# Kernel tuning notes

Measured on AMD Instinct MI355X. Metric: run time of the kernel, lower is better.

## Reference

```python
import jax, jax.numpy as jnp
import numpy as np

M = 5            # Anderson history size
LAM = 1e-4       # Tikhonov regularization on the Gram matrix
MAX_ITER = 50
TOL = 1e-5
BETA = 1.0
ALPHA = 0.9      # damping


def anderson(f, x0, m=M, lam=LAM, max_iter=MAX_ITER, tol=TOL, beta=BETA):
    """Anderson acceleration for fixed-point iteration (faithful to torch ref).

    x0: [bsz, L]. Variable history size n=min(k,m) is handled by masking the
    (m+1)x(m+1) system: inactive slots get an identity row -> alpha_j = 0.
    """
    bsz, L = x0.shape
    dt = x0.dtype
    F0 = f(x0)
    F1 = f(F0)
    X = jnp.zeros((bsz, m, L), dt).at[:, 0].set(x0).at[:, 1].set(F0)
    Fh = jnp.zeros((bsz, m, L), dt).at[:, 0].set(F0).at[:, 1].set(F1)
    eye_m = jnp.eye(m, dtype=dt)

    def body(carry):
        k, X, Fh, _ = carry
        n = jnp.minimum(k, m)
        active = (jnp.arange(m) < n).astype(dt)          # [m]
        G = Fh - X                                        # inactive rows are zero
        Hc = jnp.einsum('bil,bjl->bij', G, G) + lam * eye_m
        m2 = active[:, None] * active[None, :]
        # zero out inactive rows/cols, put 1 on their diagonal (=> alpha_j = 0)
        Hc = Hc * m2 + eye_m * (1.0 - active)
        H = jnp.zeros((bsz, m + 1, m + 1), dt)
        H = H.at[:, 0, 1:].set(active).at[:, 1:, 0].set(active).at[:, 1:, 1:].set(Hc)
        y = jnp.zeros((bsz, m + 1, 1), dt).at[:, 0, 0].set(1.0)
        alpha_c = jnp.linalg.solve(H, y)[:, 1:, 0]        # [bsz, m]
        xnew = beta * jnp.einsum('bm,bml->bl', alpha_c, Fh) \
             + (1.0 - beta) * jnp.einsum('bm,bml->bl', alpha_c, X)
        slot = k % m
        X = X.at[:, slot].set(xnew)
        fnew = f(xnew)
        Fh = Fh.at[:, slot].set(fnew)
        res = jnp.linalg.norm(fnew - xnew) / (1e-5 + jnp.linalg.norm(fnew))
        return (k + 1, X, Fh, res)

    def cond(carry):
        k, _, _, res = carry
        return jnp.logical_and(k < max_iter, res >= tol)

    k, X, Fh, res = jax.lax.while_loop(
        cond, body, (jnp.array(2), X, Fh, jnp.array(np.inf, dt)))
    return X[:, (k - 1) % m]


def make_f(x, maskf, W, b, alpha):
    """Damped forward step: z -> softmax_ch((1-a)z + a*Conv(mask-inject(z)))."""
    bsz, C, H, Wd = x.shape

    def f(zflat):
        z = zflat.reshape(bsz, C, H, Wd)
        zm = z * (1.0 - maskf) + maskf * x               # inject observed parts
        lin = jax.lax.conv_general_dilated(
            zm, W, window_strides=(1, 1), padding='SAME',
            dimension_numbers=('NCHW', 'OIHW', 'NCHW')) + b[None, :, None, None]
        pre = (1.0 - alpha) * z + alpha * lin
        return jax.nn.softmax(pre, axis=1).reshape(bsz, -1)

    return f


def setup_inputs() -> dict:
    key = jax.random.key(0)
    k1, k2, k3 = jax.random.split(key, 3)
    bsz, C, H, Wd = 32, 128, 32, 32
    x = jax.random.normal(k1, (bsz, C, H, Wd), jnp.float32)
    mask = jax.random.randint(k2, (bsz, 1, H, Wd), 0, 2).astype(jnp.int32)
    W = jax.random.normal(k3, (C, C, 3, 3), jnp.float32) * 0.05  # keep map contractive
    b = jnp.zeros((C,), jnp.float32)
    return {"x": x, "W": W, "b": b, "mask": mask}


def reference(x, W, b, mask):
    bsz, C, H, Wd = x.shape
    maskf = mask.astype(x.dtype)
    f = make_f(x, maskf, W, b, ALPHA)
    # z_start = softmax(zeros) over channel dim -> uniform 1/C
    z0 = jnp.full((bsz, C * H * Wd), 1.0 / C, x.dtype)
    zstar = anderson(f, z0)
    zn = f(zstar)            # one extra step, as in the torch forward
    return zn                # [bsz, C*H*W]
```

## Files before the change

### kernel.cpp

```cpp
#include <hip/hip_runtime.h>


typedef unsigned short u16;
using short8 = __attribute__((ext_vector_type(8))) short;
using f32x4  = __attribute__((ext_vector_type(4))) float;

#define SLOT 4194304

struct Ctrl { int done; int last_slot; };

__device__ __forceinline__ u16 f2bf(float f) {
  unsigned u = __builtin_bit_cast(unsigned, f);
  unsigned r = (u + 0x7FFFu + ((u >> 16) & 1u)) >> 16;
  return (u16)r;
}
__device__ __forceinline__ float bf2f(u16 h) {
  unsigned u = ((unsigned)h) << 16;
  return __builtin_bit_cast(float, u);
}

__global__ void __launch_bounds__(256) k_prepw(const float* __restrict__ W,
    u16* __restrict__ Wb, Ctrl* ctrl) {
  if (blockIdx.x == 0 && threadIdx.x == 0) { ctrl->done = 0; ctrl->last_slot = 4; }
  int t = blockIdx.x * 256 + threadIdx.x;
  int o = t >> 14;
  int rem = t & 16383;
  int cout = rem >> 7, cin = rem & 127;
  float v = W[(size_t)cout * 1152 + (size_t)cin * 9 + o];
  Wb[(size_t)o * 16384 + (size_t)cout * 128 + cin] = f2bf(v);
}

__global__ void __launch_bounds__(256) k_prepx(const float* __restrict__ x,
    u16* __restrict__ xsw) {
  int t = blockIdx.x * 256 + threadIdx.x;
  int g = t >> 15, p = t & 32767;
  int nb = p >> 10, gp = p & 1023, px = p & 31;
  short8 xv;
#pragma unroll
  for (int u = 0; u < 8; ++u) {
    float v = x[(size_t)nb * 131072 + (size_t)(g * 8 + u) * 1024 + gp];
    xv[u] = (short)f2bf(v);
  }
  *(short8*)(xsw + (size_t)p * 128 + (size_t)((g ^ (px & 7)) << 3)) = xv;
}

__global__ void __launch_bounds__(256)
__attribute__((amdgpu_waves_per_eu(4, 4)))
k_iter(
    const int e,
    const u16* __restrict__ xsw, const int* __restrict__ mask_,
    const u16* __restrict__ Wb, const float* __restrict__ bias,
    float* __restrict__ Fhp, u16* __restrict__ FhH, u16* __restrict__ Gp,
    float* __restrict__ gram, float* __restrict__ gpart,
    float* __restrict__ resp, Ctrl* __restrict__ ctrl)
{
  __shared__ char smem[27776];
  char*  As       = smem;
  float* rowmax_s = (float*)(smem + 26112);
  float* rowsum_s = (float*)(smem + 26624);
  float* red      = (float*)(smem + 27136);
  float* alpha_s  = (float*)(smem + 27264);
  float* res_s    = (float*)(smem + 27284);
  int*   mk3      = (int*)(smem + 27392);

  if (ctrl->done) return;

  const int tid = threadIdx.x;
  const int wv = tid >> 6, lane = tid & 63;
  const int lhi = lane >> 4, llo = lane & 15;
  const int bhw = blockIdx.x;
  const int lbid = ((bhw & 7) << 7) + (bhw >> 3);
  const int n = lbid >> 5, y0 = lbid & 31;
  const int gpix0 = (n << 10) + (y0 << 5);
  const int slot = e % 5;
  const int nact = e < 5 ? e : 5;
  const size_t base = ((size_t)lbid * 256 + tid) * 16;

  if (e >= 3) {
    if (tid < 64) {
      float sd = 0.f, sf = 0.f;
      for (int i = tid; i < 1024; i += 64) { sd += resp[2 * i]; sf += resp[2 * i + 1]; }
#pragma unroll
      for (int off = 1; off < 64; off <<= 1) { sd += __shfl_xor(sd, off); sf += __shfl_xor(sf, off); }
      if (tid == 0) res_s[0] = sqrtf(sd) / (1e-5f + sqrtf(sf));
    }
    __syncthreads();
    if (res_s[0] < 1e-5f) {
      if (tid == 0) { ctrl->done = 1; ctrl->last_slot = (e - 1) % 5; }
      return;
    }
  }

  if (tid < 96) {
    int r = tid >> 5, xx = tid & 31;
    int gy = y0 - 1 + r;
    mk3[tid] = ((unsigned)gy < 32u) ? mask_[(n << 10) + (gy << 5) + xx] : 0;
  }
  if (e >= 1 && tid >= 96 && tid < 101) {
    int j = tid - 96;
    float s = 0.f;
#pragma unroll
    for (int c = 0; c < 32; ++c) s += gpart[(size_t)((n << 5) + c) * 5 + j];
    int sp = (e - 1) % 5;
    gram[n * 25 + sp * 5 + j] = s;
    gram[n * 25 + j * 5 + sp] = s;
  }
  __syncthreads();
  if (e >= 2) {
    if (tid == 0) {
      float A[6][7];
      for (int i = 0; i < 5; ++i)
        for (int j = 0; j < 5; ++j)
          A[i + 1][j + 1] = (i < nact && j < nact)
              ? gram[n * 25 + i * 5 + j] + ((i == j) ? 1e-4f : 0.f)
              : ((i == j) ? 1.f : 0.f);
      A[0][0] = 0.f;
      for (int j = 0; j < 5; ++j) { float aj = (j < nact) ? 1.f : 0.f; A[0][j + 1] = aj; A[j + 1][0] = aj; }
      A[0][6] = 1.f;
      for (int i = 1; i < 6; ++i) A[i][6] = 0.f;
      for (int c = 0; c < 6; ++c) {
        int p = c; float mx = fabsf(A[c][c]);
        for (int r = c + 1; r < 6; ++r) { float v = fabsf(A[r][c]); if (v > mx) { mx = v; p = r; } }
        if (p != c) for (int q = c; q < 7; ++q) { float tmp = A[c][q]; A[c][q] = A[p][q]; A[p][q] = tmp; }
        float piv = A[c][c];
        for (int r = c + 1; r < 6; ++r) {
          float fr = A[r][c] / piv;
          for (int q = c; q < 7; ++q) A[r][q] -= fr * A[c][q];
        }
      }
      float sol[6];
      for (int r = 5; r >= 0; --r) {
        float s = A[r][6];
        for (int q = r + 1; q < 6; ++q) s -= A[r][q] * sol[q];
        sol[r] = s / A[r][r];
      }
      for (int j = 0; j < 5; ++j) alpha_s[j] = sol[j + 1];
    }
  } else if (tid < 5) {
    alpha_s[tid] = (tid == 0) ? 1.f : 0.f;
  }
  __syncthreads();

  float a0 = 1.f, a1 = 0.f, a2 = 0.f, a3 = 0.f, a4 = 0.f;
  if (e >= 1) { a0 = alpha_s[0]; a1 = alpha_s[1]; a2 = alpha_s[2]; a3 = alpha_s[3]; a4 = alpha_s[4]; }

#pragma unroll
  for (int uu = 0; uu < 4; ++uu) {
    int u = (uu << 8) + tid;
    int row3 = u >> 9;
    int gy = y0 - 1 + (row3 << 1);
    int idx = u & 511;
    int px = idx >> 4, grp = idx & 15;
    char* dst = As + (row3 << 1) * 8704 + ((px + 1) << 8) + ((grp ^ (px & 7)) << 4);
    short8 w = {0, 0, 0, 0, 0, 0, 0, 0};
    if ((unsigned)gy < 32u) {
      int gpix = (n << 10) + (gy << 5) + px;
      size_t off = (size_t)gpix * 128 + (size_t)((grp ^ (px & 7)) << 3);
      if (mk3[(row3 << 6) + px]) {
        w = *(const short8*)(xsw + off);
      } else if (e == 0) {
#pragma unroll
        for (int i = 0; i < 8; ++i) w[i] = (short)0x3C00;
      } else {
        short8 h0, h1, h2, h3, h4;
        h0 = *(const short8*)(FhH + off);
        if (nact > 1) h1 = *(const short8*)(FhH + SLOT + off);
        if (nact > 2) h2 = *(const short8*)(FhH + 2 * (size_t)SLOT + off);
        if (nact > 3) h3 = *(const short8*)(FhH + 3 * (size_t)SLOT + off);
        if (nact > 4) h4 = *(const short8*)(FhH + 4 * (size_t)SLOT + off);
        f32x4 va, vb;
#pragma unroll
        for (int i = 0; i < 4; ++i) { va[i] = a0 * bf2f((u16)h0[i]); vb[i] = a0 * bf2f((u16)h0[4 + i]); }
        if (nact > 1) {
#pragma unroll
          for (int i = 0; i < 4; ++i) { va[i] += a1 * bf2f((u16)h1[i]); vb[i] += a1 * bf2f((u16)h1[4 + i]); }
        }
        if (nact > 2) {
#pragma unroll
          for (int i = 0; i < 4; ++i) { va[i] += a2 * bf2f((u16)h2[i]); vb[i] += a2 * bf2f((u16)h2[4 + i]); }
        }
        if (nact > 3) {
#pragma unroll
          for (int i = 0; i < 4; ++i) { va[i] += a3 * bf2f((u16)h3[i]); vb[i] += a3 * bf2f((u16)h3[4 + i]); }
        }
        if (nact > 4) {
#pragma unroll
          for (int i = 0; i < 4; ++i) { va[i] += a4 * bf2f((u16)h4[i]); vb[i] += a4 * bf2f((u16)h4[4 + i]); }
        }
#pragma unroll
        for (int i = 0; i < 4; ++i) { w[i] = (short)f2bf(va[i]); w[4 + i] = (short)f2bf(vb[i]); }
      }
    }
    *(short8*)dst = w;
  }

  f32x4 zv[4];
  if (e == 0) {
    const f32x4 cz = {0.0078125f, 0.0078125f, 0.0078125f, 0.0078125f};
    zv[0] = cz; zv[1] = cz; zv[2] = cz; zv[3] = cz;
  } else {
    const float* fb = Fhp + base;
    f32x4 t0[4], t1[4], t2[4], t3[4], t4[4];
#pragma unroll
    for (int q = 0; q < 4; ++q) t0[q] = *(const f32x4*)(fb + q * 4);
    if (nact > 1) {
#pragma unroll
      for (int q = 0; q < 4; ++q) t1[q] = *(const f32x4*)(fb + SLOT + q * 4);
    }
    if (nact > 2) {
#pragma unroll
      for (int q = 0; q < 4; ++q) t2[q] = *(const f32x4*)(fb + 2 * SLOT + q * 4);
    }
    if (nact > 3) {
#pragma unroll
      for (int q = 0; q < 4; ++q) t3[q] = *(const f32x4*)(fb + 3 * SLOT + q * 4);
    }
    if (nact > 4) {
#pragma unroll
      for (int q = 0; q < 4; ++q) t4[q] = *(const f32x4*)(fb + 4 * SLOT + q * 4);
    }
#pragma unroll
    for (int q = 0; q < 4; ++q) zv[q] = a0 * t0[q];
    if (nact > 1) {
#pragma unroll
      for (int q = 0; q < 4; ++q) zv[q] += a1 * t1[q];
    }
    if (nact > 2) {
#pragma unroll
      for (int q = 0; q < 4; ++q) zv[q] += a2 * t2[q];
    }
    if (nact > 3) {
#pragma unroll
      for (int q = 0; q < 4; ++q) zv[q] += a3 * t3[q];
    }
    if (nact > 4) {
#pragma unroll
      for (int q = 0; q < 4; ++q) zv[q] += a4 * t4[q];
    }
  }

#pragma unroll
  for (int m2 = 0; m2 < 2; ++m2)
#pragma unroll
    for (int nf = 0; nf < 2; ++nf)
#pragma unroll
      for (int rr = 0; rr < 4; ++rr) {
        int p = (m2 << 4) + (lhi << 2) + rr;
        int ch = (wv << 5) + (nf << 4) + llo;
        int sg = (ch >> 3) ^ (p & 7);
        u16 w;
        if (mk3[32 + p])
          w = xsw[(size_t)(gpix0 + p) * 128 + (sg << 3) + (ch & 7)];
        else
          w = f2bf(zv[(m2 << 1) + nf][rr]);
        *(u16*)(As + 8704 + ((p + 1) << 8) + (sg << 4) + ((ch & 7) << 1)) = w;
      }

  if (tid < 96) {
    int r = tid >> 5, cc = tid & 31;
    int col = (cc < 16) ? 0 : 33, gc = cc & 15;
    f32x4 zz = {0.f, 0.f, 0.f, 0.f};
    *(f32x4*)(As + r * 8704 + (col << 8) + (gc << 4)) = zz;
  }
  __syncthreads();

  f32x4 acc[2][2];
  {
    const f32x4 z4 = {0.f, 0.f, 0.f, 0.f};
    acc[0][0] = z4; acc[0][1] = z4; acc[1][0] = z4; acc[1][1] = z4;
  }
#pragma unroll
  for (int o = 0; o < 9; ++o) {
    const int dy = o / 3, dx = o % 3;
    short8 bfr[2][4];
#pragma unroll
    for (int nf = 0; nf < 2; ++nf)
#pragma unroll
      for (int kk = 0; kk < 4; ++kk) {
        int ch = (wv << 5) + (nf << 4) + llo;
        bfr[nf][kk] = *(const short8*)(Wb + o * 16384 + ch * 128 + ((kk << 2) + lhi) * 8);
      }
#pragma unroll
    for (int kk = 0; kk < 4; ++kk) {
      const int kg = (kk << 2) + lhi;
#pragma unroll
      for (int m2 = 0; m2 < 2; ++m2) {
        int p = (m2 << 4) + llo;
        int cl = p + dx;
        int sg = kg ^ ((cl - 1) & 7);
        short8 af = *(const short8*)(As + dy * 8704 + (cl << 8) + (sg << 4));
#pragma unroll
        for (int nf = 0; nf < 2; ++nf)
          acc[m2][nf] = __builtin_amdgcn_mfma_f32_16x16x32_bf16(af, bfr[nf][kk], acc[m2][nf], 0, 0, 0);
      }
    }
  }

  const float bc0 = bias[(wv << 5) + llo];
  const float bc1 = bias[(wv << 5) + 16 + llo];
#pragma unroll
  for (int m2 = 0; m2 < 2; ++m2)
#pragma unroll
    for (int rr = 0; rr < 4; ++rr) {
      acc[m2][0][rr] = 0.1f * zv[m2 << 1][rr] + 0.9f * (acc[m2][0][rr] + bc0);
      acc[m2][1][rr] = 0.1f * zv[(m2 << 1) + 1][rr] + 0.9f * (acc[m2][1][rr] + bc1);
    }
#pragma unroll
  for (int m2 = 0; m2 < 2; ++m2)
#pragma unroll
    for (int rr = 0; rr < 4; ++rr) {
      float v = fmaxf(acc[m2][0][rr], acc[m2][1][rr]);
      v = fmaxf(v, __shfl_xor(v, 1)); v = fmaxf(v, __shfl_xor(v, 2));
      v = fmaxf(v, __shfl_xor(v, 4)); v = fmaxf(v, __shfl_xor(v, 8));
      if (llo == 0) rowmax_s[(((m2 << 4) + (lhi << 2) + rr) << 2) + wv] = v;
    }
  __syncthreads();
#pragma unroll
  for (int m2 = 0; m2 < 2; ++m2)
#pragma unroll
    for (int rr = 0; rr < 4; ++rr) {
      int p = (m2 << 4) + (lhi << 2) + rr;
      f32x4 m0 = *(const f32x4*)&rowmax_s[p << 2];
      float M = fmaxf(fmaxf(m0[0], m0[1]), fmaxf(m0[2], m0[3]));
      float e0 = __expf(acc[m2][0][rr] - M);
      float e1 = __expf(acc[m2][1][rr] - M);
      acc[m2][0][rr] = e0; acc[m2][1][rr] = e1;
      float s = e0 + e1;
      s += __shfl_xor(s, 1); s += __shfl_xor(s, 2);
      s += __shfl_xor(s, 4); s += __shfl_xor(s, 8);
      if (llo == 0) rowsum_s[(p << 2) + wv] = s;
    }
  __syncthreads();

  float sd = 0.f, sf = 0.f;
#pragma unroll
  for (int m2 = 0; m2 < 2; ++m2) {
    f32x4 fr0, fr1;
#pragma unroll
    for (int rr = 0; rr < 4; ++rr) {
      int p = (m2 << 4) + (lhi << 2) + rr;
      f32x4 s0 = *(const f32x4*)&rowsum_s[p << 2];
      float S = s0[0] + s0[1] + s0[2] + s0[3];
      float invS = 1.0f / S;
      float f0 = acc[m2][0][rr] * invS;
      float f1 = acc[m2][1][rr] * invS;
      acc[m2][0][rr] = f0; acc[m2][1][rr] = f1;
      fr0[rr] = f0; fr1[rr] = f1;
      float g0 = f0 - zv[m2 << 1][rr];
      float g1 = f1 - zv[(m2 << 1) + 1][rr];
      sd += g0 * g0 + g1 * g1; sf += f0 * f0 + f1 * f1;
      int ch0 = (wv << 5) + llo, ch1 = ch0 + 16;
      size_t rb = (size_t)slot * SLOT + (size_t)(gpix0 + p) * 128;
      FhH[rb + ((((ch0 >> 3) ^ (p & 7)) << 3) | (ch0 & 7))] = f2bf(f0);
      FhH[rb + ((((ch1 >> 3) ^ (p & 7)) << 3) | (ch1 & 7))] = f2bf(f1);
    }
    *(f32x4*)(Fhp + (size_t)slot * SLOT + base + (m2 << 3)) = fr0;
    *(f32x4*)(Fhp + (size_t)slot * SLOT + base + (m2 << 3) + 4) = fr1;
  }
  {
    short8 h0, h1;
#pragma unroll
    for (int m2 = 0; m2 < 2; ++m2)
#pragma unroll
      for (int nf = 0; nf < 2; ++nf)
#pragma unroll
        for (int rr = 0; rr < 4; ++rr) {
          int q = (((m2 << 1) + nf) << 2) + rr;
          u16 gb16 = f2bf(acc[m2][nf][rr] - zv[(m2 << 1) + nf][rr]);
          if (q < 8) h0[q] = (short)gb16; else h1[q - 8] = (short)gb16;
        }
    u16* Gs = Gp + (size_t)slot * SLOT + base;
    *(short8*)(Gs) = h0;
    *(short8*)(Gs + 8) = h1;
    const int jmax = e < 4 ? e : 4;
    short8 qa[5], qb[5];
#pragma unroll
    for (int j = 0; j < 5; ++j) {
      if (j != slot && j <= jmax) {
        qa[j] = *(const short8*)(Gp + (size_t)j * SLOT + base);
        qb[j] = *(const short8*)(Gp + (size_t)j * SLOT + base + 8);
      }
    }
    float gacc[5];
#pragma unroll
    for (int j = 0; j < 5; ++j) {
      if (j > jmax) { gacc[j] = 0.f; continue; }
      if (j == slot) {
        float a = 0.f;
#pragma unroll
        for (int m2 = 0; m2 < 2; ++m2)
#pragma unroll
          for (int nf = 0; nf < 2; ++nf)
#pragma unroll
            for (int rr = 0; rr < 4; ++rr) {
              float gd = acc[m2][nf][rr] - zv[(m2 << 1) + nf][rr];
              a += gd * gd;
            }
        gacc[j] = a;
      } else {
        float a = 0.f;
#pragma unroll
        for (int m2 = 0; m2 < 2; ++m2)
#pragma unroll
          for (int nf = 0; nf < 2; ++nf)
#pragma unroll
            for (int rr = 0; rr < 4; ++rr) {
              int q = (((m2 << 1) + nf) << 2) + rr;
              float gd = acc[m2][nf][rr] - zv[(m2 << 1) + nf][rr];
              float hv = bf2f((u16)(q < 8 ? qa[j][q] : qb[j][q - 8]));
              a += gd * hv;
            }
        gacc[j] = a;
      }
    }
    float vals[7] = {gacc[0], gacc[1], gacc[2], gacc[3], gacc[4], sd, sf};
#pragma unroll
    for (int i = 0; i < 7; ++i) {
      float v = vals[i];
#pragma unroll
      for (int off = 1; off < 64; off <<= 1) v += __shfl_xor(v, off);
      if (lane == 0) red[(wv << 3) + i] = v;
    }
  }
  __syncthreads();
  if (tid < 7) {
    float s = 0.f;
#pragma unroll
    for (int w = 0; w < 4; ++w) s += red[(w << 3) + tid];
    if (tid < 5)       gpart[(size_t)lbid * 5 + tid] = s;
    else if (tid == 5) resp[lbid * 2] = s;
    else               resp[lbid * 2 + 1] = s;
  }
}

__global__ void __launch_bounds__(256) k_out(const float* __restrict__ Fhp,
    const Ctrl* __restrict__ ctrl, float* __restrict__ out)
{
  __shared__ float T[32 * 132];
  int slot = ctrl->last_slot;
  const int tid = threadIdx.x;
  const int wv = tid >> 6, lane = tid & 63;
  const int lhi = lane >> 4, llo = lane & 15;
  const int lbid = blockIdx.x;
  const int n = lbid >> 5, y0 = lbid & 31;
  const size_t base = (size_t)slot * SLOT + ((size_t)lbid * 256 + tid) * 16;
#pragma unroll
  for (int m2 = 0; m2 < 2; ++m2)
#pragma unroll
    for (int nf = 0; nf < 2; ++nf) {
      f32x4 v = *(const f32x4*)(Fhp + base + (((m2 << 1) + nf) << 2));
#pragma unroll
      for (int rr = 0; rr < 4; ++rr) {
        int p = (m2 << 4) + (lhi << 2) + rr;
        int ch = (wv << 5) + (nf << 4) + llo;
        T[p * 132 + ch] = v[rr];
      }
    }
  __syncthreads();
  int c = tid >> 1, h = tid & 1;
  float* ob = out + (((size_t)(n << 7) + c) << 10) + (y0 << 5) + (h << 4);
#pragma unroll
  for (int i2 = 0; i2 < 4; ++i2) {
    f32x4 v;
#pragma unroll
    for (int i = 0; i < 4; ++i) v[i] = T[((h << 4) + (i2 << 2) + i) * 132 + c];
    *(f32x4*)(ob + (i2 << 2)) = v;
  }
}

extern "C" void kernel_launch(void* const* d_in, const int* in_sizes, int n_in,
                              void* d_out, int out_size, void* d_ws, size_t ws_size,
                              hipStream_t stream) {
  const float* x    = (const float*)d_in[0];
  const float* W    = (const float*)d_in[1];
  const float* bias = (const float*)d_in[2];
  const int*   mask = (const int*)d_in[3];
  float* out = (float*)d_out;
  char* ws = (char*)d_ws;

  float* Fhp   = (float*)(ws + 0);
  u16*   FhH   = (u16*)(ws + 83886080);
  u16*   Gp    = (u16*)(ws + 125829120);
  u16*   xsw   = (u16*)(ws + 167772160);
  u16*   Wb    = (u16*)(ws + 176160768);
  float* gram  = (float*)(ws + 176455680);
  float* gpart = (float*)(ws + 176458880);
  float* resp  = (float*)(ws + 176479360);
  Ctrl*  ctrl  = (Ctrl*)(ws + 176487552);

  k_prepw<<<576, 256, 0, stream>>>(W, Wb, ctrl);
  k_prepx<<<2048, 256, 0, stream>>>(x, xsw);
  for (int e = 0; e < 50; ++e)
    k_iter<<<1024, 256, 0, stream>>>(e, xsw, mask, Wb, bias,
                                     Fhp, FhH, Gp, gram, gpart, resp, ctrl);
  k_out<<<1024, 256, 0, stream>>>(Fhp, ctrl, out);
  (void)in_sizes; (void)n_in; (void)out_size; (void)ws_size;
}
```

Before: 422.3 us.

## Fuse Anderson iterations into one persistent kernel with a hierarchical grid barrier

Replaces the 50 per-iteration launches plus the output kernel with a single persistent kernel. The kernel loops over iterations internally and synchronises all 1024 blocks through a two-level atomic counter barrier with a generation flag. The output transpose is done in-kernel after convergence. This removes launch overhead and the early-exit launches that follow convergence. It relies on all 1024 blocks being co-resident (4 waves per EU), otherwise the barrier deadlocks, and the spin-waiting adds its own cost.

```diff
diff --git a/kernel.cpp b/kernel.cpp
--- a/kernel.cpp
+++ b/kernel.cpp
@@ -6,8 +6,6 @@
 using f32x4  = __attribute__((ext_vector_type(4))) float;
 
 #define SLOT 4194304
-
-struct Ctrl { int done; int last_slot; };
 
 __device__ __forceinline__ u16 f2bf(float f) {
   unsigned u = __builtin_bit_cast(unsigned, f);
@@ -20,8 +18,7 @@
 }
 
 __global__ void __launch_bounds__(256) k_prepw(const float* __restrict__ W,
-    u16* __restrict__ Wb, Ctrl* ctrl) {
-  if (blockIdx.x == 0 && threadIdx.x == 0) { ctrl->done = 0; ctrl->last_slot = 4; }
+    u16* __restrict__ Wb) {
   int t = blockIdx.x * 256 + threadIdx.x;
   int o = t >> 14;
   int rem = t & 16383;
@@ -46,13 +43,14 @@
 
 __global__ void __launch_bounds__(256)
 __attribute__((amdgpu_waves_per_eu(4, 4)))
-k_iter(
-    const int e,
+k_loop(
     const u16* __restrict__ xsw, const int* __restrict__ mask_,
     const u16* __restrict__ Wb, const float* __restrict__ bias,
     float* __restrict__ Fhp, u16* __restrict__ FhH, u16* __restrict__ Gp,
     float* __restrict__ gram, float* __restrict__ gpart,
-    float* __restrict__ resp, Ctrl* __restrict__ ctrl)
+    float* __restrict__ resp, unsigned* __restrict__ gen,
+    unsigned* __restrict__ gcnt, unsigned* __restrict__ cnt2,
+    float* __restrict__ out)
 {
   __shared__ char smem[27776];
   char*  As       = smem;
@@ -63,182 +61,395 @@
   float* res_s    = (float*)(smem + 27284);
   int*   mk3      = (int*)(smem + 27392);
 
-  if (ctrl->done) return;
-
   const int tid = threadIdx.x;
   const int wv = tid >> 6, lane = tid & 63;
   const int lhi = lane >> 4, llo = lane & 15;
   const int bhw = blockIdx.x;
   const int lbid = ((bhw & 7) << 7) + (bhw >> 3);
   const int n = lbid >> 5, y0 = lbid & 31;
+  const int grp = lbid >> 5;
   const int gpix0 = (n << 10) + (y0 << 5);
-  const int slot = e % 5;
-  const int nact = e < 5 ? e : 5;
   const size_t base = ((size_t)lbid * 256 + tid) * 16;
-
-  if (e >= 3) {
-    if (tid < 64) {
-      float sd = 0.f, sf = 0.f;
-      for (int i = tid; i < 1024; i += 64) { sd += resp[2 * i]; sf += resp[2 * i + 1]; }
-#pragma unroll
-      for (int off = 1; off < 64; off <<= 1) { sd += __shfl_xor(sd, off); sf += __shfl_xor(sf, off); }
-      if (tid == 0) res_s[0] = sqrtf(sd) / (1e-5f + sqrtf(sf));
-    }
-    __syncthreads();
-    if (res_s[0] < 1e-5f) {
-      if (tid == 0) { ctrl->done = 1; ctrl->last_slot = (e - 1) % 5; }
-      return;
-    }
-  }
 
   if (tid < 96) {
     int r = tid >> 5, xx = tid & 31;
     int gy = y0 - 1 + r;
     mk3[tid] = ((unsigned)gy < 32u) ? mask_[(n << 10) + (gy << 5) + xx] : 0;
+    int col = ((xx & 15) < 8) ? 0 : 33, gc = ((xx & 15) & 7) * 2 + (xx >> 4);
+    (void)col; (void)gc;
   }
-  if (e >= 1 && tid >= 96 && tid < 101) {
-    int j = tid - 96;
-    float s = 0.f;
-#pragma unroll
-    for (int c = 0; c < 32; ++c) s += gpart[(size_t)((n << 5) + c) * 5 + j];
-    int sp = (e - 1) % 5;
-    gram[n * 25 + sp * 5 + j] = s;
-    gram[n * 25 + j * 5 + sp] = s;
+  if (tid < 192) {
+    int r = tid / 64, cc = tid & 63;
+    int col = (cc < 32) ? 0 : 33, gc = cc & 31;
+    if (gc < 16) {
+      f32x4 zz = {0.f, 0.f, 0.f, 0.f};
+      *(f32x4*)(As + r * 8704 + (col << 8) + (gc << 4)) = zz;
+    }
   }
   __syncthreads();
-  if (e >= 2) {
+
+  f32x4 acc[2][2];
+  int e;
+  for (e = 0; e < 50; ++e) {
+    const int slot = e % 5;
+    const int nact = e < 5 ? e : 5;
+
+    if (e >= 3) {
+      if (tid < 64) {
+        float sd = 0.f, sf = 0.f;
+        for (int i = tid; i < 1024; i += 64) { sd += resp[2 * i]; sf += resp[2 * i + 1]; }
+#pragma unroll
+        for (int off = 1; off < 64; off <<= 1) { sd += __shfl_xor(sd, off); sf += __shfl_xor(sf, off); }
+        if (tid == 0) res_s[0] = sqrtf(sd) / (1e-5f + sqrtf(sf));
+      }
+      __syncthreads();
+      if (res_s[0] < 1e-5f) break;
+    }
+
+    if (e >= 1 && tid >= 96 && tid < 101) {
+      int j = tid - 96;
+      float s = 0.f;
+#pragma unroll
+      for (int c = 0; c < 32; ++c) s += gpart[(size_t)((n << 5) + c) * 5 + j];
+      int sp = (e - 1) % 5;
+      gram[n * 25 + sp * 5 + j] = s;
+      gram[n * 25 + j * 5 + sp] = s;
+    }
+    __syncthreads();
+    if (e >= 2) {
+      if (tid == 0) {
+        float A[6][7];
+        for (int i = 0; i < 5; ++i)
+          for (int j = 0; j < 5; ++j)
+            A[i + 1][j + 1] = (i < nact && j < nact)
+                ? gram[n * 25 + i * 5 + j] + ((i == j) ? 1e-4f : 0.f)
+                : ((i == j) ? 1.f : 0.f);
+        A[0][0] = 0.f;
+        for (int j = 0; j < 5; ++j) { float aj = (j < nact) ? 1.f : 0.f; A[0][j + 1] = aj; A[j + 1][0] = aj; }
+        A[0][6] = 1.f;
+        for (int i = 1; i < 6; ++i) A[i][6] = 0.f;
+        for (int c = 0; c < 6; ++c) {
+          int p = c; float mx = fabsf(A[c][c]);
+          for (int r = c + 1; r < 6; ++r) { float v = fabsf(A[r][c]); if (v > mx) { mx = v; p = r; } }
+          if (p != c) for (int q = c; q < 7; ++q) { float tmp = A[c][q]; A[c][q] = A[p][q]; A[p][q] = tmp; }
+          float piv = A[c][c];
+          for (int r = c + 1; r < 6; ++r) {
+            float fr = A[r][c] / piv;
+            for (int q = c; q < 7; ++q) A[r][q] -= fr * A[c][q];
+          }
+        }
+        float sol[6];
+        for (int r = 5; r >= 0; --r) {
+          float s = A[r][6];
+          for (int q = r + 1; q < 6; ++q) s -= A[r][q] * sol[q];
+          sol[r] = s / A[r][r];
+        }
+        for (int j = 0; j < 5; ++j) alpha_s[j] = sol[j + 1];
+      }
+    } else if (tid < 5) {
+      alpha_s[tid] = (tid == 0) ? 1.f : 0.f;
+    }
+    __syncthreads();
+
+    float a0 = 1.f, a1 = 0.f, a2 = 0.f, a3 = 0.f, a4 = 0.f;
+    if (e >= 1) { a0 = alpha_s[0]; a1 = alpha_s[1]; a2 = alpha_s[2]; a3 = alpha_s[3]; a4 = alpha_s[4]; }
+
+#pragma unroll
+    for (int uu = 0; uu < 4; ++uu) {
+      int u = (uu << 8) + tid;
+      int row3 = u >> 9;
+      int gy = y0 - 1 + (row3 << 1);
+      int idx = u & 511;
+      int px = idx >> 4, gq = idx & 15;
+      char* dst = As + (row3 << 1) * 8704 + ((px + 1) << 8) + ((gq ^ (px & 7)) << 4);
+      short8 w = {0, 0, 0, 0, 0, 0, 0, 0};
+      if ((unsigned)gy < 32u) {
+        int gpix = (n << 10) + (gy << 5) + px;
+        size_t off = (size_t)gpix * 128 + (size_t)((gq ^ (px & 7)) << 3);
+        if (mk3[(row3 << 6) + px]) {
+          w = *(const short8*)(xsw + off);
+        } else if (e == 0) {
+#pragma unroll
+          for (int i = 0; i < 8; ++i) w[i] = (short)0x3C00;
+        } else {
+          short8 h0, h1, h2, h3, h4;
+          h0 = *(const short8*)(FhH + off);
+          if (nact > 1) h1 = *(const short8*)(FhH + SLOT + off);
+          if (nact > 2) h2 = *(const short8*)(FhH + 2 * (size_t)SLOT + off);
+          if (nact > 3) h3 = *(const short8*)(FhH + 3 * (size_t)SLOT + off);
+          if (nact > 4) h4 = *(const short8*)(FhH + 4 * (size_t)SLOT + off);
+          f32x4 va, vb;
+#pragma unroll
+          for (int i = 0; i < 4; ++i) { va[i] = a0 * bf2f((u16)h0[i]); vb[i] = a0 * bf2f((u16)h0[4 + i]); }
+          if (nact > 1) {
+#pragma unroll
+            for (int i = 0; i < 4; ++i) { va[i] += a1 * bf2f((u16)h1[i]); vb[i] += a1 * bf2f((u16)h1[4 + i]); }
+          }
+          if (nact > 2) {
+#pragma unroll
+            for (int i = 0; i < 4; ++i) { va[i] += a2 * bf2f((u16)h2[i]); vb[i] += a2 * bf2f((u16)h2[4 + i]); }
+          }
+          if (nact > 3) {
+#pragma unroll
+            for (int i = 0; i < 4; ++i) { va[i] += a3 * bf2f((u16)h3[i]); vb[i] += a3 * bf2f((u16)h3[4 + i]); }
+          }
+          if (nact > 4) {
+#pragma unroll
+            for (int i = 0; i < 4; ++i) { va[i] += a4 * bf2f((u16)h4[i]); vb[i] += a4 * bf2f((u16)h4[4 + i]); }
+          }
+#pragma unroll
+          for (int i = 0; i < 4; ++i) { w[i] = (short)f2bf(va[i]); w[4 + i] = (short)f2bf(vb[i]); }
+        }
+      }
+      *(short8*)dst = w;
+    }
+
+    f32x4 zv[4];
+    if (e == 0) {
+      const f32x4 cz = {0.0078125f, 0.0078125f, 0.0078125f, 0.0078125f};
+      zv[0] = cz; zv[1] = cz; zv[2] = cz; zv[3] = cz;
+    } else {
+      const float* fb = Fhp + base;
+      f32x4 t0[4], t1[4], t2[4], t3[4], t4[4];
+#pragma unroll
+      for (int q = 0; q < 4; ++q) t0[q] = *(const f32x4*)(fb + q * 4);
+      if (nact > 1) {
+#pragma unroll
+        for (int q = 0; q < 4; ++q) t1[q] = *(const f32x4*)(fb + SLOT + q * 4);
+      }
+      if (nact > 2) {
+#pragma unroll
+        for (int q = 0; q < 4; ++q) t2[q] = *(const f32x4*)(fb + 2 * SLOT + q * 4);
+      }
+      if (nact > 3) {
+#pragma unroll
+        for (int q = 0; q < 4; ++q) t3[q] = *(const f32x4*)(fb + 3 * SLOT + q * 4);
+      }
+      if (nact > 4) {
+#pragma unroll
+        for (int q = 0; q < 4; ++q) t4[q] = *(const f32x4*)(fb + 4 * SLOT + q * 4);
+      }
+#pragma unroll
+      for (int q = 0; q < 4; ++q) zv[q] = a0 * t0[q];
+      if (nact > 1) {
+#pragma unroll
+        for (int q = 0; q < 4; ++q) zv[q] += a1 * t1[q];
+      }
+      if (nact > 2) {
+#pragma unroll
+        for (int q = 0; q < 4; ++q) zv[q] += a2 * t2[q];
+      }
+      if (nact > 3) {
+#pragma unroll
+        for (int q = 0; q < 4; ++q) zv[q] += a3 * t3[q];
+      }
+      if (nact > 4) {
+#pragma unroll
+        for (int q = 0; q < 4; ++q) zv[q] += a4 * t4[q];
+      }
+    }
+
+#pragma unroll
+    for (int m2 = 0; m2 < 2; ++m2)
+#pragma unroll
+      for (int nf = 0; nf < 2; ++nf)
+#pragma unroll
+        for (int rr = 0; rr < 4; ++rr) {
+          int p = (m2 << 4) + (lhi << 2) + rr;
+          int ch = (wv << 5) + (nf << 4) + llo;
+          int sg = (ch >> 3) ^ (p & 7);
+          u16 w;
+          if (mk3[32 + p])
+            w = xsw[(size_t)(gpix0 + p) * 128 + (sg << 3) + (ch & 7)];
+          else
+            w = f2bf(zv[(m2 << 1) + nf][rr]);
+          *(u16*)(As + 8704 + ((p + 1) << 8) + (sg << 4) + ((ch & 7) << 1)) = w;
+        }
+    __syncthreads();
+
+    {
+      const f32x4 z4 = {0.f, 0.f, 0.f, 0.f};
+      acc[0][0] = z4; acc[0][1] = z4; acc[1][0] = z4; acc[1][1] = z4;
+    }
+#pragma unroll
+    for (int o = 0; o < 9; ++o) {
+      const int dy = o / 3, dx = o % 3;
+      short8 bfr[2][4];
+#pragma unroll
+      for (int nf = 0; nf < 2; ++nf)
+#pragma unroll
+        for (int kk = 0; kk < 4; ++kk) {
+          int ch = (wv << 5) + (nf << 4) + llo;
+          bfr[nf][kk] = *(const short8*)(Wb + o * 16384 + ch * 128 + ((kk << 2) + lhi) * 8);
+        }
+#pragma unroll
+      for (int kk = 0; kk < 4; ++kk) {
+        const int kg = (kk << 2) + lhi;
+#pragma unroll
+        for (int m2 = 0; m2 < 2; ++m2) {
+          int p = (m2 << 4) + llo;
+          int cl = p + dx;
+          int sg = kg ^ ((cl - 1) & 7);
+          short8 af = *(const short8*)(As + dy * 8704 + (cl << 8) + (sg << 4));
+#pragma unroll
+          for (int nf = 0; nf < 2; ++nf)
+            acc[m2][nf] = __builtin_amdgcn_mfma_f32_16x16x32_bf16(af, bfr[nf][kk], acc[m2][nf], 0, 0, 0);
+        }
+      }
+    }
+
+    const float bc0 = bias[(wv << 5) + llo];
+    const float bc1 = bias[(wv << 5) + 16 + llo];
+#pragma unroll
+    for (int m2 = 0; m2 < 2; ++m2)
+#pragma unroll
+      for (int rr = 0; rr < 4; ++rr) {
+        acc[m2][0][rr] = 0.1f * zv[m2 << 1][rr] + 0.9f * (acc[m2][0][rr] + bc0);
+        acc[m2][1][rr] = 0.1f * zv[(m2 << 1) + 1][rr] + 0.9f * (acc[m2][1][rr] + bc1);
+      }
+#pragma unroll
+    for (int m2 = 0; m2 < 2; ++m2)
+#pragma unroll
+      for (int rr = 0; rr < 4; ++rr) {
+        float v = fmaxf(acc[m2][0][rr], acc[m2][1][rr]);
+        v = fmaxf(v, __shfl_xor(v, 1)); v = fmaxf(v, __shfl_xor(v, 2));
+        v = fmaxf(v, __shfl_xor(v, 4)); v = fmaxf(v, __shfl_xor(v, 8));
+        if (llo == 0) rowmax_s[(((m2 << 4) + (lhi << 2) + rr) << 2) + wv] = v;
+      }
+    __syncthreads();
+#pragma unroll
+    for (int m2 = 0; m2 < 2; ++m2)
+#pragma unroll
+      for (int rr = 0; rr < 4; ++rr) {
+        int p = (m2 << 4) + (lhi << 2) + rr;
+        f32x4 m0 = *(const f32x4*)&rowmax_s[p << 2];
+        float M = fmaxf(fmaxf(m0[0], m0[1]), fmaxf(m0[2], m0[3]));
+        float e0 = __expf(acc[m2][0][rr] - M);
+        float e1 = __expf(acc[m2][1][rr] - M);
+        acc[m2][0][rr] = e0; acc[m2][1][rr] = e1;
+        float s = e0 + e1;
+        s += __shfl_xor(s, 1); s += __shfl_xor(s, 2);
+        s += __shfl_xor(s, 4); s += __shfl_xor(s, 8);
+        if (llo == 0) rowsum_s[(p << 2) + wv] = s;
+      }
+    __syncthreads();
+
+    float sd = 0.f, sf = 0.f;
+#pragma unroll
+    for (int m2 = 0; m2 < 2; ++m2) {
+      f32x4 fr0, fr1;
+#pragma unroll
+      for (int rr = 0; rr < 4; ++rr) {
+        int p = (m2 << 4) + (lhi << 2) + rr;
+        f32x4 s0 = *(const f32x4*)&rowsum_s[p << 2];
+        float S = s0[0] + s0[1] + s0[2] + s0[3];
+        float invS = 1.0f / S;
+        float f0 = acc[m2][0][rr] * invS;
+        float f1 = acc[m2][1][rr] * invS;
+        acc[m2][0][rr] = f0; acc[m2][1][rr] = f1;
+        fr0[rr] = f0; fr1[rr] = f1;
+        float g0 = f0 - zv[m2 << 1][rr];
+        float g1 = f1 - zv[(m2 << 1) + 1][rr];
+        sd += g0 * g0 + g1 * g1; sf += f0 * f0 + f1 * f1;
+        int ch0 = (wv << 5) + llo, ch1 = ch0 + 16;
+        size_t rb = (size_t)slot * SLOT + (size_t)(gpix0 + p) * 128;
+        FhH[rb + ((((ch0 >> 3) ^ (p & 7)) << 3) | (ch0 & 7))] = f2bf(f0);
+        FhH[rb + ((((ch1 >> 3) ^ (p & 7)) << 3) | (ch1 & 7))] = f2bf(f1);
+      }
+      *(f32x4*)(Fhp + (size_t)slot * SLOT + base + (m2 << 3)) = fr0;
+      *(f32x4*)(Fhp + (size_t)slot * SLOT + base + (m2 << 3) + 4) = fr1;
+    }
+    {
+      short8 h0, h1;
+#pragma unroll
+      for (int m2 = 0; m2 < 2; ++m2)
+#pragma unroll
+        for (int nf = 0; nf < 2; ++nf)
+#pragma unroll
+          for (int rr = 0; rr < 4; ++rr) {
+            int q = (((m2 << 1) + nf) << 2) + rr;
+            u16 gb16 = f2bf(acc[m2][nf][rr] - zv[(m2 << 1) + nf][rr]);
+            if (q < 8) h0[q] = (short)gb16; else h1[q - 8] = (short)gb16;
+          }
+      u16* Gs = Gp + (size_t)slot * SLOT + base;
+      *(short8*)(Gs) = h0;
+      *(short8*)(Gs + 8) = h1;
+      const int jmax = e < 4 ? e : 4;
+      short8 qa[5], qb[5];
+#pragma unroll
+      for (int j = 0; j < 5; ++j) {
+        if (j != slot && j <= jmax) {
+          qa[j] = *(const short8*)(Gp + (size_t)j * SLOT + base);
+          qb[j] = *(const short8*)(Gp + (size_t)j * SLOT + base + 8);
+        }
+      }
+      float gacc[5];
+#pragma unroll
+      for (int j = 0; j < 5; ++j) {
+        if (j > jmax) { gacc[j] = 0.f; continue; }
+        float a = 0.f;
+        if (j == slot) {
+#pragma unroll
+          for (int m2 = 0; m2 < 2; ++m2)
+#pragma unroll
+            for (int nf = 0; nf < 2; ++nf)
+#pragma unroll
+              for (int rr = 0; rr < 4; ++rr) {
+                float gd = acc[m2][nf][rr] - zv[(m2 << 1) + nf][rr];
+                a += gd * gd;
+              }
+        } else {
+#pragma unroll
+          for (int m2 = 0; m2 < 2; ++m2)
+#pragma unroll
+            for (int nf = 0; nf < 2; ++nf)
+#pragma unroll
+              for (int rr = 0; rr < 4; ++rr) {
+                int q = (((m2 << 1) + nf) << 2) + rr;
+                float gd = acc[m2][nf][rr] - zv[(m2 << 1) + nf][rr];
+                float hv = bf2f((u16)(q < 8 ? qa[j][q] : qb[j][q - 8]));
+                a += gd * hv;
+              }
+        }
+        gacc[j] = a;
+      }
+      float vals[7] = {gacc[0], gacc[1], gacc[2], gacc[3], gacc[4], sd, sf};
+#pragma unroll
+      for (int i = 0; i < 7; ++i) {
+        float v = vals[i];
+#pragma unroll
+        for (int off = 1; off < 64; off <<= 1) v += __shfl_xor(v, off);
+        if (lane == 0) red[(wv << 3) + i] = v;
+      }
+    }
+    __syncthreads();
+    if (tid < 7) {
+      float s = 0.f;
+#pragma unroll
+      for (int w = 0; w < 4; ++w) s += red[(w << 3) + tid];
+      if (tid < 5)       gpart[(size_t)lbid * 5 + tid] = s;
+      else if (tid == 5) resp[lbid * 2] = s;
+      else               resp[lbid * 2 + 1] = s;
+    }
+
+    __syncthreads();
     if (tid == 0) {
-      float A[6][7];
-      for (int i = 0; i < 5; ++i)
-        for (int j = 0; j < 5; ++j)
-          A[i + 1][j + 1] = (i < nact && j < nact)
-              ? gram[n * 25 + i * 5 + j] + ((i == j) ? 1e-4f : 0.f)
-              : ((i == j) ? 1.f : 0.f);
-      A[0][0] = 0.f;
-      for (int j = 0; j < 5; ++j) { float aj = (j < nact) ? 1.f : 0.f; A[0][j + 1] = aj; A[j + 1][0] = aj; }
-      A[0][6] = 1.f;
-      for (int i = 1; i < 6; ++i) A[i][6] = 0.f;
-      for (int c = 0; c < 6; ++c) {
-        int p = c; float mx = fabsf(A[c][c]);
-        for (int r = c + 1; r < 6; ++r) { float v = fabsf(A[r][c]); if (v > mx) { mx = v; p = r; } }
-        if (p != c) for (int q = c; q < 7; ++q) { float tmp = A[c][q]; A[c][q] = A[p][q]; A[p][q] = tmp; }
-        float piv = A[c][c];
-        for (int r = c + 1; r < 6; ++r) {
-          float fr = A[r][c] / piv;
-          for (int q = c; q < 7; ++q) A[r][q] -= fr * A[c][q];
-        }
-      }
-      float sol[6];
-      for (int r = 5; r >= 0; --r) {
-        float s = A[r][6];
-        for (int q = r + 1; q < 6; ++q) s -= A[r][q] * sol[q];
-        sol[r] = s / A[r][r];
-      }
-      for (int j = 0; j < 5; ++j) alpha_s[j] = sol[j + 1];
-    }
-  } else if (tid < 5) {
-    alpha_s[tid] = (tid == 0) ? 1.f : 0.f;
+      __threadfence();
+      if (atomicAdd(&gcnt[(e << 5) + grp], 1u) == 31u) {
+        if (atomicAdd(&cnt2[e], 1u) == 31u)
+          __hip_atomic_store(gen, (unsigned)(e + 1), __ATOMIC_RELEASE,
+                             __HIP_MEMORY_SCOPE_AGENT);
+      }
+      while (__hip_atomic_load(gen, __ATOMIC_RELAXED,
+                               __HIP_MEMORY_SCOPE_AGENT) <= (unsigned)e)
+        __builtin_amdgcn_s_sleep(2);
+      __threadfence();
+    }
+    __syncthreads();
   }
+
   __syncthreads();
-
-  float a0 = 1.f, a1 = 0.f, a2 = 0.f, a3 = 0.f, a4 = 0.f;
-  if (e >= 1) { a0 = alpha_s[0]; a1 = alpha_s[1]; a2 = alpha_s[2]; a3 = alpha_s[3]; a4 = alpha_s[4]; }
-
-#pragma unroll
-  for (int uu = 0; uu < 4; ++uu) {
-    int u = (uu << 8) + tid;
-    int row3 = u >> 9;
-    int gy = y0 - 1 + (row3 << 1);
-    int idx = u & 511;
-    int px = idx >> 4, grp = idx & 15;
-    char* dst = As + (row3 << 1) * 8704 + ((px + 1) << 8) + ((grp ^ (px & 7)) << 4);
-    short8 w = {0, 0, 0, 0, 0, 0, 0, 0};
-    if ((unsigned)gy < 32u) {
-      int gpix = (n << 10) + (gy << 5) + px;
-      size_t off = (size_t)gpix * 128 + (size_t)((grp ^ (px & 7)) << 3);
-      if (mk3[(row3 << 6) + px]) {
-        w = *(const short8*)(xsw + off);
-      } else if (e == 0) {
-#pragma unroll
-        for (int i = 0; i < 8; ++i) w[i] = (short)0x3C00;
-      } else {
-        short8 h0, h1, h2, h3, h4;
-        h0 = *(const short8*)(FhH + off);
-        if (nact > 1) h1 = *(const short8*)(FhH + SLOT + off);
-        if (nact > 2) h2 = *(const short8*)(FhH + 2 * (size_t)SLOT + off);
-        if (nact > 3) h3 = *(const short8*)(FhH + 3 * (size_t)SLOT + off);
-        if (nact > 4) h4 = *(const short8*)(FhH + 4 * (size_t)SLOT + off);
-        f32x4 va, vb;
-#pragma unroll
-        for (int i = 0; i < 4; ++i) { va[i] = a0 * bf2f((u16)h0[i]); vb[i] = a0 * bf2f((u16)h0[4 + i]); }
-        if (nact > 1) {
-#pragma unroll
-          for (int i = 0; i < 4; ++i) { va[i] += a1 * bf2f((u16)h1[i]); vb[i] += a1 * bf2f((u16)h1[4 + i]); }
-        }
-        if (nact > 2) {
-#pragma unroll
-          for (int i = 0; i < 4; ++i) { va[i] += a2 * bf2f((u16)h2[i]); vb[i] += a2 * bf2f((u16)h2[4 + i]); }
-        }
-        if (nact > 3) {
-#pragma unroll
-          for (int i = 0; i < 4; ++i) { va[i] += a3 * bf2f((u16)h3[i]); vb[i] += a3 * bf2f((u16)h3[4 + i]); }
-        }
-        if (nact > 4) {
-#pragma unroll
-          for (int i = 0; i < 4; ++i) { va[i] += a4 * bf2f((u16)h4[i]); vb[i] += a4 * bf2f((u16)h4[4 + i]); }
-        }
-#pragma unroll
-        for (int i = 0; i < 4; ++i) { w[i] = (short)f2bf(va[i]); w[4 + i] = (short)f2bf(vb[i]); }
-      }
-    }
-    *(short8*)dst = w;
-  }
-
-  f32x4 zv[4];
-  if (e == 0) {
-    const f32x4 cz = {0.0078125f, 0.0078125f, 0.0078125f, 0.0078125f};
-    zv[0] = cz; zv[1] = cz; zv[2] = cz; zv[3] = cz;
-  } else {
-    const float* fb = Fhp + base;
-    f32x4 t0[4], t1[4], t2[4], t3[4], t4[4];
-#pragma unroll
-    for (int q = 0; q < 4; ++q) t0[q] = *(const f32x4*)(fb + q * 4);
-    if (nact > 1) {
-#pragma unroll
-      for (int q = 0; q < 4; ++q) t1[q] = *(const f32x4*)(fb + SLOT + q * 4);
-    }
-    if (nact > 2) {
-#pragma unroll
-      for (int q = 0; q < 4; ++q) t2[q] = *(const f32x4*)(fb + 2 * SLOT + q * 4);
-    }
-    if (nact > 3) {
-#pragma unroll
-      for (int q = 0; q < 4; ++q) t3[q] = *(const f32x4*)(fb + 3 * SLOT + q * 4);
-    }
-    if (nact > 4) {
-#pragma unroll
-      for (int q = 0; q < 4; ++q) t4[q] = *(const f32x4*)(fb + 4 * SLOT + q * 4);
-    }
-#pragma unroll
-    for (int q = 0; q < 4; ++q) zv[q] = a0 * t0[q];
-    if (nact > 1) {
-#pragma unroll
-      for (int q = 0; q < 4; ++q) zv[q] += a1 * t1[q];
-    }
-    if (nact > 2) {
-#pragma unroll
-      for (int q = 0; q < 4; ++q) zv[q] += a2 * t2[q];
-    }
-    if (nact > 3) {
-#pragma unroll
-      for (int q = 0; q < 4; ++q) zv[q] += a3 * t3[q];
-    }
-    if (nact > 4) {
-#pragma unroll
-      for (int q = 0; q < 4; ++q) zv[q] += a4 * t4[q];
-    }
-  }
-
+  float* T = (float*)smem;
 #pragma unroll
   for (int m2 = 0; m2 < 2; ++m2)
 #pragma unroll
@@ -247,224 +458,19 @@
       for (int rr = 0; rr < 4; ++rr) {
         int p = (m2 << 4) + (lhi << 2) + rr;
         int ch = (wv << 5) + (nf << 4) + llo;
-        int sg = (ch >> 3) ^ (p & 7);
-        u16 w;
-        if (mk3[32 + p])
-          w = xsw[(size_t)(gpix0 + p) * 128 + (sg << 3) + (ch & 7)];
-        else
-          w = f2bf(zv[(m2 << 1) + nf][rr]);
-        *(u16*)(As + 8704 + ((p + 1) << 8) + (sg << 4) + ((ch & 7) << 1)) = w;
-      }
-
-  if (tid < 96) {
-    int r = tid >> 5, cc = tid & 31;
-    int col = (cc < 16) ? 0 : 33, gc = cc & 15;
-    f32x4 zz = {0.f, 0.f, 0.f, 0.f};
-    *(f32x4*)(As + r * 8704 + (col << 8) + (gc << 4)) = zz;
-  }
+        T[p * 132 + ch] = acc[m2][nf][rr];
+      }
   __syncthreads();
-
-  f32x4 acc[2][2];
   {
-    const f32x4 z4 = {0.f, 0.f, 0.f, 0.f};
-    acc[0][0] = z4; acc[0][1] = z4; acc[1][0] = z4; acc[1][1] = z4;
-  }
-#pragma unroll
-  for (int o = 0; o < 9; ++o) {
-    const int dy = o / 3, dx = o % 3;
-    short8 bfr[2][4];
-#pragma unroll
-    for (int nf = 0; nf < 2; ++nf)
-#pragma unroll
-      for (int kk = 0; kk < 4; ++kk) {
-        int ch = (wv << 5) + (nf << 4) + llo;
-        bfr[nf][kk] = *(const short8*)(Wb + o * 16384 + ch * 128 + ((kk << 2) + lhi) * 8);
-      }
-#pragma unroll
-    for (int kk = 0; kk < 4; ++kk) {
-      const int kg = (kk << 2) + lhi;
-#pragma unroll
-      for (int m2 = 0; m2 < 2; ++m2) {
-        int p = (m2 << 4) + llo;
-        int cl = p + dx;
-        int sg = kg ^ ((cl - 1) & 7);
-        short8 af = *(const short8*)(As + dy * 8704 + (cl << 8) + (sg << 4));
-#pragma unroll
-        for (int nf = 0; nf < 2; ++nf)
-          acc[m2][nf] = __builtin_amdgcn_mfma_f32_16x16x32_bf16(af, bfr[nf][kk], acc[m2][nf], 0, 0, 0);
-      }
-    }
-  }
-
-  const float bc0 = bias[(wv << 5) + llo];
-  const float bc1 = bias[(wv << 5) + 16 + llo];
-#pragma unroll
-  for (int m2 = 0; m2 < 2; ++m2)
-#pragma unroll
-    for (int rr = 0; rr < 4; ++rr) {
-      acc[m2][0][rr] = 0.1f * zv[m2 << 1][rr] + 0.9f * (acc[m2][0][rr] + bc0);
-      acc[m2][1][rr] = 0.1f * zv[(m2 << 1) + 1][rr] + 0.9f * (acc[m2][1][rr] + bc1);
-    }
-#pragma unroll
-  for (int m2 = 0; m2 < 2; ++m2)
-#pragma unroll
-    for (int rr = 0; rr < 4; ++rr) {
-      float v = fmaxf(acc[m2][0][rr], acc[m2][1][rr]);
-      v = fmaxf(v, __shfl_xor(v, 1)); v = fmaxf(v, __shfl_xor(v, 2));
-      v = fmaxf(v, __shfl_xor(v, 4)); v = fmaxf(v, __shfl_xor(v, 8));
-      if (llo == 0) rowmax_s[(((m2 << 4) + (lhi << 2) + rr) << 2) + wv] = v;
-    }
-  __syncthreads();
-#pragma unroll
-  for (int m2 = 0; m2 < 2; ++m2)
-#pragma unroll
-    for (int rr = 0; rr < 4; ++rr) {
-      int p = (m2 << 4) + (lhi << 2) + rr;
-      f32x4 m0 = *(const f32x4*)&rowmax_s[p << 2];
-      float M = fmaxf(fmaxf(m0[0], m0[1]), fmaxf(m0[2], m0[3]));
-      float e0 = __expf(acc[m2][0][rr] - M);
-      float e1 = __expf(acc[m2][1][rr] - M);
-      acc[m2][0][rr] = e0; acc[m2][1][rr] = e1;
-      float s = e0 + e1;
-      s += __shfl_xor(s, 1); s += __shfl_xor(s, 2);
-      s += __shfl_xor(s, 4); s += __shfl_xor(s, 8);
-      if (llo == 0) rowsum_s[(p << 2) + wv] = s;
-    }
-  __syncthreads();
-
-  float sd = 0.f, sf = 0.f;
-#pragma unroll
-  for (int m2 = 0; m2 < 2; ++m2) {
-    f32x4 fr0, fr1;
-#pragma unroll
-    for (int rr = 0; rr < 4; ++rr) {
-      int p = (m2 << 4) + (lhi << 2) + rr;
-      f32x4 s0 = *(const f32x4*)&rowsum_s[p << 2];
-      float S = s0[0] + s0[1] + s0[2] + s0[3];
-      float invS = 1.0f / S;
-      float f0 = acc[m2][0][rr] * invS;
-      float f1 = acc[m2][1][rr] * invS;
-      acc[m2][0][rr] = f0; acc[m2][1][rr] = f1;
-      fr0[rr] = f0; fr1[rr] = f1;
-      float g0 = f0 - zv[m2 << 1][rr];
-      float g1 = f1 - zv[(m2 << 1) + 1][rr];
-      sd += g0 * g0 + g1 * g1; sf += f0 * f0 + f1 * f1;
-      int ch0 = (wv << 5) + llo, ch1 = ch0 + 16;
-      size_t rb = (size_t)slot * SLOT + (size_t)(gpix0 + p) * 128;
-      FhH[rb + ((((ch0 >> 3) ^ (p & 7)) << 3) | (ch0 & 7))] = f2bf(f0);
-      FhH[rb + ((((ch1 >> 3) ^ (p & 7)) << 3) | (ch1 & 7))] = f2bf(f1);
-    }
-    *(f32x4*)(Fhp + (size_t)slot * SLOT + base + (m2 << 3)) = fr0;
-    *(f32x4*)(Fhp + (size_t)slot * SLOT + base + (m2 << 3) + 4) = fr1;
-  }
-  {
-    short8 h0, h1;
-#pragma unroll
-    for (int m2 = 0; m2 < 2; ++m2)
-#pragma unroll
-      for (int nf = 0; nf < 2; ++nf)
-#pragma unroll
-        for (int rr = 0; rr < 4; ++rr) {
-          int q = (((m2 << 1) + nf) << 2) + rr;
-          u16 gb16 = f2bf(acc[m2][nf][rr] - zv[(m2 << 1) + nf][rr]);
-          if (q < 8) h0[q] = (short)gb16; else h1[q - 8] = (short)gb16;
-        }
-    u16* Gs = Gp + (size_t)slot * SLOT + base;
-    *(short8*)(Gs) = h0;
-    *(short8*)(Gs + 8) = h1;
-    const int jmax = e < 4 ? e : 4;
-    short8 qa[5], qb[5];
-#pragma unroll
-    for (int j = 0; j < 5; ++j) {
-      if (j != slot && j <= jmax) {
-        qa[j] = *(const short8*)(Gp + (size_t)j * SLOT + base);
-        qb[j] = *(const short8*)(Gp + (size_t)j * SLOT + base + 8);
-      }
-    }
-    float gacc[5];
-#pragma unroll
-    for (int j = 0; j < 5; ++j) {
-      if (j > jmax) { gacc[j] = 0.f; continue; }
-      if (j == slot) {
-        float a = 0.f;
-#pragma unroll
-        for (int m2 = 0; m2 < 2; ++m2)
-#pragma unroll
-          for (int nf = 0; nf < 2; ++nf)
-#pragma unroll
-            for (int rr = 0; rr < 4; ++rr) {
-              float gd = acc[m2][nf][rr] - zv[(m2 << 1) + nf][rr];
-              a += gd * gd;
-            }
-        gacc[j] = a;
-      } else {
-        float a = 0.f;
-#pragma unroll
-        for (int m2 = 0; m2 < 2; ++m2)
-#pragma unroll
-          for (int nf = 0; nf < 2; ++nf)
-#pragma unroll
-            for (int rr = 0; rr < 4; ++rr) {
-              int q = (((m2 << 1) + nf) << 2) + rr;
-              float gd = acc[m2][nf][rr] - zv[(m2 << 1) + nf][rr];
-              float hv = bf2f((u16)(q < 8 ? qa[j][q] : qb[j][q - 8]));
-              a += gd * hv;
-            }
-        gacc[j] = a;
-      }
-    }
-    float vals[7] = {gacc[0], gacc[1], gacc[2], gacc[3], gacc[4], sd, sf};
-#pragma unroll
-    for (int i = 0; i < 7; ++i) {
-      float v = vals[i];
-#pragma unroll
-      for (int off = 1; off < 64; off <<= 1) v += __shfl_xor(v, off);
-      if (lane == 0) red[(wv << 3) + i] = v;
-    }
-  }
-  __syncthreads();
-  if (tid < 7) {
-    float s = 0.f;
-#pragma unroll
-    for (int w = 0; w < 4; ++w) s += red[(w << 3) + tid];
-    if (tid < 5)       gpart[(size_t)lbid * 5 + tid] = s;
-    else if (tid == 5) resp[lbid * 2] = s;
-    else               resp[lbid * 2 + 1] = s;
-  }
-}
-
-__global__ void __launch_bounds__(256) k_out(const float* __restrict__ Fhp,
-    const Ctrl* __restrict__ ctrl, float* __restrict__ out)
-{
-  __shared__ float T[32 * 132];
-  int slot = ctrl->last_slot;
-  const int tid = threadIdx.x;
-  const int wv = tid >> 6, lane = tid & 63;
-  const int lhi = lane >> 4, llo = lane & 15;
-  const int lbid = blockIdx.x;
-  const int n = lbid >> 5, y0 = lbid & 31;
-  const size_t base = (size_t)slot * SLOT + ((size_t)lbid * 256 + tid) * 16;
-#pragma unroll
-  for (int m2 = 0; m2 < 2; ++m2)
-#pragma unroll
-    for (int nf = 0; nf < 2; ++nf) {
-      f32x4 v = *(const f32x4*)(Fhp + base + (((m2 << 1) + nf) << 2));
-#pragma unroll
-      for (int rr = 0; rr < 4; ++rr) {
-        int p = (m2 << 4) + (lhi << 2) + rr;
-        int ch = (wv << 5) + (nf << 4) + llo;
-        T[p * 132 + ch] = v[rr];
-      }
-    }
-  __syncthreads();
-  int c = tid >> 1, h = tid & 1;
-  float* ob = out + (((size_t)(n << 7) + c) << 10) + (y0 << 5) + (h << 4);
-#pragma unroll
-  for (int i2 = 0; i2 < 4; ++i2) {
-    f32x4 v;
-#pragma unroll
-    for (int i = 0; i < 4; ++i) v[i] = T[((h << 4) + (i2 << 2) + i) * 132 + c];
-    *(f32x4*)(ob + (i2 << 2)) = v;
+    int c = tid >> 1, xs = (tid & 1) << 4;
+    float* ob = out + (((size_t)(n << 7) + c) << 10) + (y0 << 5) + xs;
+#pragma unroll
+    for (int i2 = 0; i2 < 4; ++i2) {
+      f32x4 v;
+#pragma unroll
+      for (int i = 0; i < 4; ++i) v[i] = T[(xs + (i2 << 2) + i) * 132 + c];
+      *(f32x4*)(ob + (i2 << 2)) = v;
+    }
   }
 }
 
@@ -478,21 +484,22 @@
   float* out = (float*)d_out;
   char* ws = (char*)d_ws;
 
-  float* Fhp   = (float*)(ws + 0);
-  u16*   FhH   = (u16*)(ws + 83886080);
-  u16*   Gp    = (u16*)(ws + 125829120);
-  u16*   xsw   = (u16*)(ws + 167772160);
-  u16*   Wb    = (u16*)(ws + 176160768);
-  float* gram  = (float*)(ws + 176455680);
-  float* gpart = (float*)(ws + 176458880);
-  float* resp  = (float*)(ws + 176479360);
-  Ctrl*  ctrl  = (Ctrl*)(ws + 176487552);
-
-  k_prepw<<<576, 256, 0, stream>>>(W, Wb, ctrl);
+  float*    Fhp  = (float*)(ws + 0);
+  u16*      FhH  = (u16*)(ws + 83886080);
+  u16*      Gp   = (u16*)(ws + 125829120);
+  u16*      xsw  = (u16*)(ws + 167772160);
+  u16*      Wb   = (u16*)(ws + 176160768);
+  float*    gram = (float*)(ws + 176455680);
+  float*    gpart= (float*)(ws + 176458880);
+  float*    resp = (float*)(ws + 176479360);
+  unsigned* gen  = (unsigned*)(ws + 176487552);
+  unsigned* gcnt = (unsigned*)(ws + 176487616);
+  unsigned* cnt2 = (unsigned*)(ws + 176494016);
+
+  hipMemsetAsync(ws + 176487552, 0, 6664, stream);
+  k_prepw<<<576, 256, 0, stream>>>(W, Wb);
   k_prepx<<<2048, 256, 0, stream>>>(x, xsw);
-  for (int e = 0; e < 50; ++e)
-    k_iter<<<1024, 256, 0, stream>>>(e, xsw, mask, Wb, bias,
-                                     Fhp, FhH, Gp, gram, gpart, resp, ctrl);
-  k_out<<<1024, 256, 0, stream>>>(Fhp, ctrl, out);
+  k_loop<<<1024, 256, 0, stream>>>(xsw, mask, Wb, bias, Fhp, FhH, Gp,
+                                   gram, gpart, resp, gen, gcnt, cnt2, out);
   (void)in_sizes; (void)n_in; (void)out_size; (void)ws_size;
 }
```

Measured after the change: 1.197 ms. 2.84x slower.
